# Performance work log

Hardware: AMD Instinct MI355X
Metric: run time of the kernel (lower is better)

The kernel has to match this reference:

```python
import jax, jax.numpy as jnp
import numpy as np

B, DC, DB, DF = 16384, 2048, 768, 256
NF = DB  # num_features (isSwinT=True)
EPS = 1e-5


def setup_inputs() -> dict:
    key = jax.random.key(0)
    ks = jax.random.split(key, 20)
    s = 0.02
    return {
        'x_context': jax.random.normal(ks[0], (B, DC), jnp.float32),
        'x_body': jax.random.normal(ks[1], (B, DB), jnp.float32),
        'x_face': jax.random.normal(ks[2], (B, DF), jnp.float32),
        'Wc': jax.random.normal(ks[3], (NF, DC), jnp.float32) * s,
        'bc': jax.random.normal(ks[4], (NF,), jnp.float32) * s,
        'Wa1': jax.random.normal(ks[5], (128, NF), jnp.float32) * s,
        'ba1': jax.random.normal(ks[6], (128,), jnp.float32) * s,
        'ga': jnp.ones((128,), jnp.float32),
        'bba': jnp.zeros((128,), jnp.float32),
        'Wa2': jax.random.normal(ks[7], (1, 128), jnp.float32) * s,
        'ba2': jax.random.normal(ks[8], (1,), jnp.float32) * s,
        'W1': jax.random.normal(ks[9], (256, NF * 3), jnp.float32) * s,
        'b1': jax.random.normal(ks[10], (256,), jnp.float32) * s,
        'g1': jnp.ones((256,), jnp.float32),
        'be1': jnp.zeros((256,), jnp.float32),
        'Wcat': jax.random.normal(ks[11], (26, 256), jnp.float32) * s,
        'bcat': jax.random.normal(ks[12], (26,), jnp.float32) * s,
    }


def _bn(x, g, b):
    # BatchNorm1d, training mode (biased batch stats), deterministic
    m = jnp.mean(x, axis=0)
    v = jnp.mean((x - m) ** 2, axis=0)
    return (x - m) * jax.lax.rsqrt(v + EPS) * g + b


def reference(x_context, x_body, x_face, Wc, bc, Wa1, ba1, ga, bba, Wa2, ba2,
              W1, b1, g1, be1, Wcat, bcat):
    # face repeated elementwise to body width: [B,256,1]->repeat(3)->view[B,768]
    face = jnp.repeat(x_face, DB // DF, axis=1)              # [B, NF]
    ctx = x_context @ Wc.T + bc                              # [B, NF]
    body = x_body                                            # [B, NF]

    def cross_atten(a, u, v):
        # two 1x1 dot-products, softmax over size-2 dim, weighted sum
        d = jnp.stack([jnp.sum(a * u, axis=1), jnp.sum(a * v, axis=1)], axis=1)  # [B,2]
        att = jax.nn.softmax(d, axis=1)
        # sum over dim2 of a[:, :, None] @ att[:, None, :] == a * att.sum(1)
        return a * jnp.sum(att, axis=1, keepdims=True)

    cfeat = cross_atten(ctx, body, face)
    bfeat = cross_atten(body, ctx, face)
    ffeat = cross_atten(face, ctx, body)

    def fc_att(x):
        h = _bn(x @ Wa1.T + ba1, ga, bba)
        h = jax.nn.gelu(h, approximate=False)
        return h @ Wa2.T + ba2                               # [B, 1]

    score = jax.nn.softmax(
        jnp.concatenate([fc_att(cfeat), fc_att(bfeat), fc_att(ffeat)], axis=1), axis=1)  # [B,3]
    cfeat = cfeat * score[:, 0:1]
    bfeat = bfeat * score[:, 1:2]
    ffeat = ffeat * score[:, 2:3]

    fuse = jnp.concatenate([cfeat, bfeat, ffeat], axis=1) @ W1.T + b1  # [B,256]
    fuse = jax.nn.relu(_bn(fuse, g1, be1))  # dropout p=0.5 treated as identity (eval)
    return fuse @ Wcat.T + bcat             # [B,26]
```

## Files before the change

kernel.cpp:

```cpp
#include <hip/hip_runtime.h>
#include <hip/hip_bf16.h>
#include <stdint.h>

typedef float f32x4 __attribute__((ext_vector_type(4)));
typedef short bf16x8 __attribute__((ext_vector_type(8)));
typedef unsigned short u16;

static constexpr int kB  = 16384;
static constexpr int kDC = 2048;
static constexpr int kNF = 768;
static constexpr float kEps = 1e-5f;

static constexpr size_t OFF_FEATS  = 0;
static constexpr size_t OFF_X      = 75497472;
static constexpr size_t OFF_WCBF   = OFF_X + 67108864;
static constexpr size_t OFF_WA1BF  = OFF_WCBF + 3145728;
static constexpr size_t OFF_W1BF   = OFF_WA1BF + 196608;
static constexpr size_t OFF_FUSE   = OFF_W1BF + 1179648;
static constexpr size_t OFF_SCORES = OFF_FUSE + 16777216;
static constexpr size_t OFF_STATS  = OFF_SCORES + 196608;

static __device__ __forceinline__ u16 f2bf(float x) {
  union { float f; unsigned u; } c; c.f = x;
  unsigned r = c.u + 0x7fffu + ((c.u >> 16) & 1u);
  return (u16)(r >> 16);
}

static __device__ __forceinline__ unsigned pk2(float lo, float hi) {
  union { __hip_bfloat162 h; unsigned u; } c;
  c.h = __float22bfloat162_rn(make_float2(lo, hi));
  return c.u;
}

static __device__ __forceinline__ void cvt4(const float* __restrict__ in, u16* __restrict__ out, long v) {
  const float4 f = ((const float4*)in)[v];
  ((ushort4*)out)[v] = make_ushort4(f2bf(f.x), f2bf(f.y), f2bf(f.z), f2bf(f.w));
}

__global__ __launch_bounds__(256) void prep_kernel(
    const float* __restrict__ xb, const float* __restrict__ xf,
    const float* __restrict__ Wc, const float* __restrict__ Wa1, const float* __restrict__ W1,
    u16* __restrict__ feats, u16* __restrict__ wcbf, u16* __restrict__ wa1bf, u16* __restrict__ w1bf)
{
  const int b = blockIdx.x, t = threadIdx.x;
  if (b < 3072) {
    const long base = (long)b * 1024 + t;
    u16* o = feats + (size_t)kB * kNF;
#pragma unroll
    for (int i = 0; i < 4; ++i) cvt4(xb, o, base + i * 256);
  } else if (b < 4096) {
    const long base = (long)(b - 3072) * 1024 + t;
#pragma unroll
    for (int i = 0; i < 4; ++i) {
      const long v = base + i * 256;
      const float4 f = ((const float4*)xf)[v];
      u16 e0 = f2bf(f.x), e1 = f2bf(f.y), e2 = f2bf(f.z), e3 = f2bf(f.w);
      size_t p = (size_t)v * 4;
      size_t row = p >> 8;
      int col = (int)(p & 255);
      u16* o = feats + (size_t)2 * kB * kNF + row * kNF + col * 3;
      ushort4* o4 = (ushort4*)o;
      o4[0] = make_ushort4(e0, e0, e0, e1);
      o4[1] = make_ushort4(e1, e1, e2, e2);
      o4[2] = make_ushort4(e2, e3, e3, e3);
    }
  } else if (b < 4480) {
    const long base = (long)(b - 4096) * 1024 + t;
#pragma unroll
    for (int i = 0; i < 4; ++i) cvt4(Wc, wcbf, base + i * 256);
  } else if (b < 4504) {
    const long base = (long)(b - 4480) * 1024 + t;
#pragma unroll
    for (int i = 0; i < 4; ++i) cvt4(Wa1, wa1bf, base + i * 256);
  } else {
    const long base = (long)(b - 4504) * 1024 + t;
#pragma unroll
    for (int i = 0; i < 4; ++i) cvt4(W1, w1bf, base + i * 256);
  }
}

static __device__ __forceinline__ void gload16(const void* g, void* l) {
  __builtin_amdgcn_global_load_lds(
      (const __attribute__((address_space(1))) void*)g,
      (__attribute__((address_space(3))) void*)l, 16, 0, 0);
}

__global__ __launch_bounds__(256) void gemm_a32(
    const float* __restrict__ A, const u16* __restrict__ B,
    const float* __restrict__ bias, u16* __restrict__ C)
{
  constexpr int APAD = 40;
  __shared__ __align__(16) u16 As[2 * 128 * APAD];
  __shared__ __align__(16) u16 Bs[2 * 128 * 32];
  const int bx = blockIdx.x, by = blockIdx.y;
  const size_t m0 = (size_t)bx * 128;
  const int n0 = by * 128;
  const int t = threadIdx.x;
  const int lane = t & 63, wave = t >> 6;
  const int wm = (wave >> 1) * 64, wn = (wave & 1) * 64;
  const int fr = lane & 15, fq = lane >> 4;

  const int srow = t >> 2, scol = (t & 3) * 8;
  const u16* gb0 = B + (size_t)(n0 + srow) * kDC + scol;
  const u16* gb1 = B + (size_t)(n0 + 64 + srow) * kDC + scol;

  const int arow = t >> 1, ah = (t & 1);
  const float* ga = A + (m0 + arow) * (size_t)kDC + ah * 16;
  const int lawoff = arow * APAD + ah * 16;

  float4 ra0, ra1, ra2, ra3;
  auto loadA = [&]() {
    ra0 = ((const float4*)ga)[0]; ra1 = ((const float4*)ga)[1];
    ra2 = ((const float4*)ga)[2]; ra3 = ((const float4*)ga)[3];
  };
  auto cvtWrite = [&](u16* dst) {
    uint4 w0, w1;
    w0.x = pk2(ra0.x, ra0.y); w0.y = pk2(ra0.z, ra0.w);
    w0.z = pk2(ra1.x, ra1.y); w0.w = pk2(ra1.z, ra1.w);
    w1.x = pk2(ra2.x, ra2.y); w1.y = pk2(ra2.z, ra2.w);
    w1.z = pk2(ra3.x, ra3.y); w1.w = pk2(ra3.z, ra3.w);
    ((uint4*)dst)[0] = w0; ((uint4*)dst)[1] = w1;
  };

  f32x4 acc[4][4] = {};

  loadA();
  cvtWrite(As + lawoff);
  gload16(gb0, Bs + t * 8);
  gload16(gb1, Bs + t * 8 + 2048);
  gb0 += 32; gb1 += 32;
  ga += 32; loadA();
  __syncthreads();

  for (int k = 0; k < 64; ++k) {
    const int cur = k & 1;
    if (k < 63) {
      u16* an = As + (cur ^ 1) * (128 * APAD);
      u16* bn = Bs + (cur ^ 1) * (128 * 32);
      cvtWrite(an + lawoff);
      gload16(gb0, bn + t * 8);
      gload16(gb1, bn + t * 8 + 2048);
      gb0 += 32; gb1 += 32;
      if (k < 62) { ga += 32; loadA(); }
    }
    const u16* fa = As + cur * (128 * APAD) + (wm + fr) * APAD + fq * 8;
    const u16* fb = Bs + cur * (128 * 32) + (wn + fr) * 32 + fq * 8;
    bf16x8 av[4], bv[4];
#pragma unroll
    for (int mf = 0; mf < 4; ++mf) av[mf] = *(const bf16x8*)(fa + mf * 16 * APAD);
#pragma unroll
    for (int nf = 0; nf < 4; ++nf) bv[nf] = *(const bf16x8*)(fb + nf * 512);
#pragma unroll
    for (int mf = 0; mf < 4; ++mf)
#pragma unroll
      for (int nf = 0; nf < 4; ++nf)
        acc[mf][nf] = __builtin_amdgcn_mfma_f32_16x16x32_bf16(av[mf], bv[nf], acc[mf][nf], 0, 0, 0);
    __syncthreads();
  }

#pragma unroll
  for (int mf = 0; mf < 4; ++mf) {
    const size_t rb = m0 + wm + mf * 16 + fq * 4;
#pragma unroll
    for (int nf = 0; nf < 4; ++nf) {
      const int gn = n0 + wn + nf * 16 + fr;
      const float bb = bias[gn];
#pragma unroll
      for (int rr = 0; rr < 4; ++rr)
        C[(rb + rr) * (size_t)kNF + gn] = f2bf(acc[mf][nf][rr] + bb);
    }
  }
}

template <int STATS>
__global__ __launch_bounds__(256) void gemm_bt64(
    const u16* __restrict__ A, int lda, const u16* __restrict__ B, int ldb,
    const float* __restrict__ bias, float* __restrict__ C, int ldc, int K,
    float* __restrict__ stats)
{
  __shared__ __align__(16) u16 As[2 * 64 * 32];
  __shared__ __align__(16) u16 Bs[2 * 128 * 32];
  const int bx = blockIdx.x, by = blockIdx.y;
  const size_t m0 = (size_t)bx * 64;
  const int n0 = by * 128;
  const int t = threadIdx.x;
  const int lane = t & 63, wave = t >> 6;
  const int wn = wave * 32;
  const int fr = lane & 15, fq = lane >> 4;

  const int srow = t >> 2, scol = (t & 3) * 8;
  const u16* ga0 = A + (m0 + srow) * (size_t)lda + scol;
  const u16* gb0 = B + (size_t)(n0 + srow) * ldb + scol;
  const u16* gb1 = B + (size_t)(n0 + 64 + srow) * ldb + scol;

  f32x4 acc[4][2] = {};

  gload16(ga0, As + t * 8);
  gload16(gb0, Bs + t * 8);
  gload16(gb1, Bs + t * 8 + 2048);
  ga0 += 32; gb0 += 32; gb1 += 32;
  __syncthreads();

  const int kt = K >> 5;
  for (int k = 0; k < kt; ++k) {
    const int cur = k & 1;
    if (k + 1 < kt) {
      u16* an = As + (cur ^ 1) * 2048;
      u16* bn = Bs + (cur ^ 1) * 4096;
      gload16(ga0, an + t * 8);
      gload16(gb0, bn + t * 8);
      gload16(gb1, bn + t * 8 + 2048);
      ga0 += 32; gb0 += 32; gb1 += 32;
    }
    const u16* fa = As + cur * 2048 + fr * 32 + fq * 8;
    const u16* fb = Bs + cur * 4096 + (wn + fr) * 32 + fq * 8;
    bf16x8 av[4], bv[2];
#pragma unroll
    for (int mf = 0; mf < 4; ++mf) av[mf] = *(const bf16x8*)(fa + mf * 512);
#pragma unroll
    for (int nf = 0; nf < 2; ++nf) bv[nf] = *(const bf16x8*)(fb + nf * 512);
#pragma unroll
    for (int mf = 0; mf < 4; ++mf)
#pragma unroll
      for (int nf = 0; nf < 2; ++nf)
        acc[mf][nf] = __builtin_amdgcn_mfma_f32_16x16x32_bf16(av[mf], bv[nf], acc[mf][nf], 0, 0, 0);
    __syncthreads();
  }

  float cs[2] = {}, cs2[2] = {};
#pragma unroll
  for (int mf = 0; mf < 4; ++mf) {
    const size_t rb = m0 + mf * 16 + fq * 4;
#pragma unroll
    for (int nf = 0; nf < 2; ++nf) {
      const int gn = n0 + wn + nf * 16 + fr;
      const float bb = bias[gn];
#pragma unroll
      for (int rr = 0; rr < 4; ++rr) {
        const float vv = acc[mf][nf][rr] + bb;
        C[(rb + rr) * (size_t)ldc + gn] = vv;
        if (STATS) { cs[nf] += vv; cs2[nf] += vv * vv; }
      }
    }
  }
  if (STATS) {
    const int f = (int)(m0 >> 14);
#pragma unroll
    for (int nf = 0; nf < 2; ++nf) {
      float s = cs[nf], s2 = cs2[nf];
      s += __shfl_down(s, 32); s2 += __shfl_down(s2, 32);
      s += __shfl_down(s, 16); s2 += __shfl_down(s2, 16);
      if (fq == 0) {
        const int gn = n0 + wn + nf * 16 + fr;
        atomicAdd(&stats[(f * 128 + gn) * 2 + 0], s);
        atomicAdd(&stats[(f * 128 + gn) * 2 + 1], s2);
      }
    }
  }
}

__global__ __launch_bounds__(256) void gemm_fuse64(
    const u16* __restrict__ feats, const u16* __restrict__ w1,
    const float* __restrict__ scores, const float* __restrict__ b1,
    float* __restrict__ fuse, float* __restrict__ fstats)
{
  __shared__ __align__(16) u16 As[2 * 64 * 32];
  __shared__ __align__(16) u16 Bs[2 * 128 * 32];
  const int bx = blockIdx.x, by = blockIdx.y;
  const size_t m0 = (size_t)bx * 64;
  const int n0 = by * 128;
  const int t = threadIdx.x;
  const int lane = t & 63, wave = t >> 6;
  const int wn = wave * 32;
  const int fr = lane & 15, fq = lane >> 4;
  const int srow = t >> 2, scol = (t & 3) * 8;

  const u16* ga0; const u16* gb0; const u16* gb1;
  auto setf = [&](int f) {
    ga0 = feats + (size_t)f * kB * kNF + (m0 + srow) * (size_t)kNF + scol;
    gb0 = w1 + f * kNF + (size_t)(n0 + srow) * 2304 + scol;
    gb1 = gb0 + (size_t)64 * 2304;
  };

  const f32x4 vzero = {};
  f32x4 acc[4][2] = {}, tot[4][2] = {};

  setf(0);
  gload16(ga0, As + t * 8);
  gload16(gb0, Bs + t * 8);
  gload16(gb1, Bs + t * 8 + 2048);
  ga0 += 32; gb0 += 32; gb1 += 32;
  int pf = 0, pk = 1;
  int ck = 0, cf = 0;
  __syncthreads();

  for (int s = 0; s < 72; ++s) {
    const int cur = s & 1;
    if (s < 71) {
      u16* an = As + (cur ^ 1) * 2048;
      u16* bn = Bs + (cur ^ 1) * 4096;
      gload16(ga0, an + t * 8);
      gload16(gb0, bn + t * 8);
      gload16(gb1, bn + t * 8 + 2048);
      if (++pk == 24) { pk = 0; ++pf; if (pf < 3) setf(pf); }
      else { ga0 += 32; gb0 += 32; gb1 += 32; }
    }
    const u16* fa = As + cur * 2048 + fr * 32 + fq * 8;
    const u16* fb = Bs + cur * 4096 + (wn + fr) * 32 + fq * 8;
    bf16x8 av[4], bv[2];
#pragma unroll
    for (int mf = 0; mf < 4; ++mf) av[mf] = *(const bf16x8*)(fa + mf * 512);
#pragma unroll
    for (int nf = 0; nf < 2; ++nf) bv[nf] = *(const bf16x8*)(fb + nf * 512);
#pragma unroll
    for (int mf = 0; mf < 4; ++mf)
#pragma unroll
      for (int nf = 0; nf < 2; ++nf)
        acc[mf][nf] = __builtin_amdgcn_mfma_f32_16x16x32_bf16(av[mf], bv[nf], acc[mf][nf], 0, 0, 0);
    if (++ck == 24) {
      ck = 0;
#pragma unroll
      for (int mf = 0; mf < 4; ++mf) {
        const size_t rb = m0 + mf * 16 + fq * 4;
#pragma unroll
        for (int rr = 0; rr < 4; ++rr) {
          const float sv = scores[(rb + rr) * 3 + cf];
#pragma unroll
          for (int nf = 0; nf < 2; ++nf) tot[mf][nf][rr] += sv * acc[mf][nf][rr];
        }
      }
#pragma unroll
      for (int mf = 0; mf < 4; ++mf)
#pragma unroll
        for (int nf = 0; nf < 2; ++nf) acc[mf][nf] = vzero;
      ++cf;
    }
    __syncthreads();
  }

  float cs[2] = {}, cs2[2] = {};
#pragma unroll
  for (int mf = 0; mf < 4; ++mf) {
    const size_t rb = m0 + mf * 16 + fq * 4;
#pragma unroll
    for (int nf = 0; nf < 2; ++nf) {
      const int gn = n0 + wn + nf * 16 + fr;
      const float bb = b1[gn];
#pragma unroll
      for (int rr = 0; rr < 4; ++rr) {
        const float vv = tot[mf][nf][rr] + bb;
        fuse[(rb + rr) * 256 + gn] = vv;
        cs[nf] += vv; cs2[nf] += vv * vv;
      }
    }
  }
#pragma unroll
  for (int nf = 0; nf < 2; ++nf) {
    float s = cs[nf], s2 = cs2[nf];
    s += __shfl_down(s, 32); s2 += __shfl_down(s2, 32);
    s += __shfl_down(s, 16); s2 += __shfl_down(s2, 16);
    if (fq == 0) {
      const int gn = n0 + wn + nf * 16 + fr;
      atomicAdd(&fstats[gn * 2 + 0], s);
      atomicAdd(&fstats[gn * 2 + 1], s2);
    }
  }
}

__global__ __launch_bounds__(64) void att_kernel(
    const float* __restrict__ H, const float* __restrict__ stats,
    const float* __restrict__ ga, const float* __restrict__ bba,
    const float* __restrict__ Wa2, const float* __restrict__ ba2,
    float* __restrict__ scores)
{
  const int i = blockIdx.x, l = threadIdx.x;
  float d[3];
#pragma unroll
  for (int f = 0; f < 3; ++f) {
    float part = 0.f;
#pragma unroll
    for (int h = 0; h < 2; ++h) {
      const int c = l + h * 64;
      const float sum = stats[(f * 128 + c) * 2 + 0];
      const float sq  = stats[(f * 128 + c) * 2 + 1];
      const float m = sum * (1.f / kB);
      const float var = sq * (1.f / kB) - m * m;
      const float rs = rsqrtf(var + kEps);
      const float x = H[((size_t)f * kB + i) * 128 + c];
      const float xn = (x - m) * rs * ga[c] + bba[c];
      const float ge = 0.5f * xn * (1.f + erff(xn * 0.70710678118f));
      part += ge * Wa2[c];
    }
#pragma unroll
    for (int off = 32; off > 0; off >>= 1) part += __shfl_down(part, off);
    d[f] = part;
  }
  if (l == 0) {
    const float b2 = ba2[0];
    float d0 = d[0] + b2, d1 = d[1] + b2, d2 = d[2] + b2;
    const float mx = fmaxf(d0, fmaxf(d1, d2));
    const float e0 = expf(d0 - mx), e1 = expf(d1 - mx), e2 = expf(d2 - mx);
    const float inv = 1.f / (e0 + e1 + e2);
    scores[i * 3 + 0] = e0 * inv;
    scores[i * 3 + 1] = e1 * inv;
    scores[i * 3 + 2] = e2 * inv;
  }
}

__global__ __launch_bounds__(64) void final_kernel(
    const float* __restrict__ fuse, const float* __restrict__ fstats,
    const float* __restrict__ g1, const float* __restrict__ be1,
    const float* __restrict__ Wcat, const float* __restrict__ bcat,
    float* __restrict__ out)
{
  const int i = blockIdx.x, l = threadIdx.x;
  __shared__ float row[256];
#pragma unroll
  for (int h = 0; h < 4; ++h) {
    const int c = l + h * 64;
    const float sum = fstats[c * 2 + 0], sq = fstats[c * 2 + 1];
    const float m = sum * (1.f / kB);
    const float var = sq * (1.f / kB) - m * m;
    const float rs = rsqrtf(var + kEps);
    const float v = (fuse[(size_t)i * 256 + c] - m) * rs * g1[c] + be1[c];
    row[c] = fmaxf(v, 0.f);
  }
  __syncthreads();
  if (l < 26) {
    float acc = bcat[l];
    const float* w = Wcat + l * 256;
    for (int k2 = 0; k2 < 256; ++k2) acc += row[k2] * w[k2];
    out[(size_t)i * 26 + l] = acc;
  }
}

extern "C" void kernel_launch(void* const* d_in, const int* in_sizes, int n_in,
                              void* d_out, int out_size, void* d_ws, size_t ws_size,
                              hipStream_t stream) {
  (void)in_sizes; (void)n_in; (void)out_size; (void)ws_size;
  const float* xc   = (const float*)d_in[0];
  const float* xb   = (const float*)d_in[1];
  const float* xf   = (const float*)d_in[2];
  const float* Wc   = (const float*)d_in[3];
  const float* bc   = (const float*)d_in[4];
  const float* Wa1  = (const float*)d_in[5];
  const float* ba1  = (const float*)d_in[6];
  const float* ga   = (const float*)d_in[7];
  const float* bba  = (const float*)d_in[8];
  const float* Wa2  = (const float*)d_in[9];
  const float* ba2  = (const float*)d_in[10];
  const float* W1   = (const float*)d_in[11];
  const float* b1   = (const float*)d_in[12];
  const float* g1   = (const float*)d_in[13];
  const float* be1  = (const float*)d_in[14];
  const float* Wcat = (const float*)d_in[15];
  const float* bcat = (const float*)d_in[16];
  float* out = (float*)d_out;

  char* ws = (char*)d_ws;
  u16* feats   = (u16*)(ws + OFF_FEATS);
  float* H     = (float*)(ws + OFF_X);
  u16* wcbf    = (u16*)(ws + OFF_WCBF);
  u16* wa1bf   = (u16*)(ws + OFF_WA1BF);
  u16* w1bf    = (u16*)(ws + OFF_W1BF);
  float* fuse  = (float*)(ws + OFF_FUSE);
  float* scores= (float*)(ws + OFF_SCORES);
  float* hst   = (float*)(ws + OFF_STATS);
  float* fst   = (float*)(ws + OFF_STATS + 3072);

  hipMemsetAsync(ws + OFF_STATS, 0, 5120, stream);
  prep_kernel<<<4648, 256, 0, stream>>>(xb, xf, Wc, Wa1, W1, feats, wcbf, wa1bf, w1bf);
  gemm_a32<<<dim3(128, 6), 256, 0, stream>>>(xc, wcbf, bc, feats);
  gemm_bt64<1><<<dim3(768, 1), 256, 0, stream>>>(feats, kNF, wa1bf, kNF, ba1, H, 128, kNF, hst);
  att_kernel<<<kB, 64, 0, stream>>>(H, hst, ga, bba, Wa2, ba2, scores);
  gemm_fuse64<<<dim3(256, 2), 256, 0, stream>>>(feats, w1bf, scores, b1, fuse, fst);
  final_kernel<<<kB, 64, 0, stream>>>(fuse, fst, g1, be1, Wcat, bcat, out);
}
```

Measured before the change: 299.8 us.

## Pre-convert x_context to bf16 and use single-buffered bf16 GEMM for context projection

Moves the fp32-to-bf16 conversion of x_context out of the context GEMM into the prep kernel, writing a bf16 copy into the workspace region later reused for H. The GEMM now loads both operands straight to LDS with global_load_lds and drops register-staged A conversion and double buffering. The prep kernel also doubles work per block. This adds an extra 128MB fp32 read plus 64MB bf16 write and read round trip, and the loss of double buffering may expose load latency.

```diff
diff --git a/kernel.cpp b/kernel.cpp
--- a/kernel.cpp
+++ b/kernel.cpp
@@ -26,32 +26,31 @@
   return (u16)(r >> 16);
 }
 
-static __device__ __forceinline__ unsigned pk2(float lo, float hi) {
-  union { __hip_bfloat162 h; unsigned u; } c;
-  c.h = __float22bfloat162_rn(make_float2(lo, hi));
-  return c.u;
-}
-
 static __device__ __forceinline__ void cvt4(const float* __restrict__ in, u16* __restrict__ out, long v) {
   const float4 f = ((const float4*)in)[v];
   ((ushort4*)out)[v] = make_ushort4(f2bf(f.x), f2bf(f.y), f2bf(f.z), f2bf(f.w));
 }
 
 __global__ __launch_bounds__(256) void prep_kernel(
-    const float* __restrict__ xb, const float* __restrict__ xf,
+    const float* __restrict__ xc, const float* __restrict__ xb, const float* __restrict__ xf,
     const float* __restrict__ Wc, const float* __restrict__ Wa1, const float* __restrict__ W1,
-    u16* __restrict__ feats, u16* __restrict__ wcbf, u16* __restrict__ wa1bf, u16* __restrict__ w1bf)
+    u16* __restrict__ axbf, u16* __restrict__ feats,
+    u16* __restrict__ wcbf, u16* __restrict__ wa1bf, u16* __restrict__ w1bf)
 {
   const int b = blockIdx.x, t = threadIdx.x;
-  if (b < 3072) {
-    const long base = (long)b * 1024 + t;
+  if (b < 4096) {
+    const long base = (long)b * 2048 + t;
+#pragma unroll
+    for (int i = 0; i < 8; ++i) cvt4(xc, axbf, base + i * 256);
+  } else if (b < 5632) {
+    const long base = (long)(b - 4096) * 2048 + t;
     u16* o = feats + (size_t)kB * kNF;
 #pragma unroll
-    for (int i = 0; i < 4; ++i) cvt4(xb, o, base + i * 256);
-  } else if (b < 4096) {
-    const long base = (long)(b - 3072) * 1024 + t;
-#pragma unroll
-    for (int i = 0; i < 4; ++i) {
+    for (int i = 0; i < 8; ++i) cvt4(xb, o, base + i * 256);
+  } else if (b < 6144) {
+    const long base = (long)(b - 5632) * 2048 + t;
+#pragma unroll
+    for (int i = 0; i < 8; ++i) {
       const long v = base + i * 256;
       const float4 f = ((const float4*)xf)[v];
       u16 e0 = f2bf(f.x), e1 = f2bf(f.y), e2 = f2bf(f.z), e3 = f2bf(f.w);
@@ -64,18 +63,18 @@
       o4[1] = make_ushort4(e1, e1, e2, e2);
       o4[2] = make_ushort4(e2, e3, e3, e3);
     }
-  } else if (b < 4480) {
-    const long base = (long)(b - 4096) * 1024 + t;
-#pragma unroll
-    for (int i = 0; i < 4; ++i) cvt4(Wc, wcbf, base + i * 256);
-  } else if (b < 4504) {
-    const long base = (long)(b - 4480) * 1024 + t;
-#pragma unroll
-    for (int i = 0; i < 4; ++i) cvt4(Wa1, wa1bf, base + i * 256);
+  } else if (b < 6336) {
+    const long base = (long)(b - 6144) * 2048 + t;
+#pragma unroll
+    for (int i = 0; i < 8; ++i) cvt4(Wc, wcbf, base + i * 256);
+  } else if (b < 6348) {
+    const long base = (long)(b - 6336) * 2048 + t;
+#pragma unroll
+    for (int i = 0; i < 8; ++i) cvt4(Wa1, wa1bf, base + i * 256);
   } else {
-    const long base = (long)(b - 4504) * 1024 + t;
-#pragma unroll
-    for (int i = 0; i < 4; ++i) cvt4(W1, w1bf, base + i * 256);
+    const long base = (long)(b - 6348) * 2048 + t;
+#pragma unroll
+    for (int i = 0; i < 8; ++i) cvt4(W1, w1bf, base + i * 256);
   }
 }
 
@@ -85,13 +84,12 @@
       (__attribute__((address_space(3))) void*)l, 16, 0, 0);
 }
 
-__global__ __launch_bounds__(256) void gemm_a32(
-    const float* __restrict__ A, const u16* __restrict__ B,
-    const float* __restrict__ bias, u16* __restrict__ C)
-{
-  constexpr int APAD = 40;
-  __shared__ __align__(16) u16 As[2 * 128 * APAD];
-  __shared__ __align__(16) u16 Bs[2 * 128 * 32];
+__global__ __launch_bounds__(256) void gemm_bt(
+    const u16* __restrict__ A, int lda, const u16* __restrict__ B, int ldb,
+    const float* __restrict__ bias, u16* __restrict__ C, int ldc, int K)
+{
+  __shared__ __align__(16) u16 As[128 * 32];
+  __shared__ __align__(16) u16 Bs[128 * 32];
   const int bx = blockIdx.x, by = blockIdx.y;
   const size_t m0 = (size_t)bx * 128;
   const int n0 = by * 128;
@@ -101,53 +99,29 @@
   const int fr = lane & 15, fq = lane >> 4;
 
   const int srow = t >> 2, scol = (t & 3) * 8;
-  const u16* gb0 = B + (size_t)(n0 + srow) * kDC + scol;
-  const u16* gb1 = B + (size_t)(n0 + 64 + srow) * kDC + scol;
-
-  const int arow = t >> 1, ah = (t & 1);
-  const float* ga = A + (m0 + arow) * (size_t)kDC + ah * 16;
-  const int lawoff = arow * APAD + ah * 16;
-
-  float4 ra0, ra1, ra2, ra3;
-  auto loadA = [&]() {
-    ra0 = ((const float4*)ga)[0]; ra1 = ((const float4*)ga)[1];
-    ra2 = ((const float4*)ga)[2]; ra3 = ((const float4*)ga)[3];
-  };
-  auto cvtWrite = [&](u16* dst) {
-    uint4 w0, w1;
-    w0.x = pk2(ra0.x, ra0.y); w0.y = pk2(ra0.z, ra0.w);
-    w0.z = pk2(ra1.x, ra1.y); w0.w = pk2(ra1.z, ra1.w);
-    w1.x = pk2(ra2.x, ra2.y); w1.y = pk2(ra2.z, ra2.w);
-    w1.z = pk2(ra3.x, ra3.y); w1.w = pk2(ra3.z, ra3.w);
-    ((uint4*)dst)[0] = w0; ((uint4*)dst)[1] = w1;
-  };
+  const u16* ga0 = A + (m0 + srow) * (size_t)lda + scol;
+  const u16* ga1 = A + (m0 + 64 + srow) * (size_t)lda + scol;
+  const u16* gb0 = B + (size_t)(n0 + srow) * ldb + scol;
+  const u16* gb1 = B + (size_t)(n0 + 64 + srow) * ldb + scol;
+  u16* la = As + t * 8;
+  u16* lb = Bs + t * 8;
+  const u16* fa = As + (wm + fr) * 32 + fq * 8;
+  const u16* fb = Bs + (wn + fr) * 32 + fq * 8;
 
   f32x4 acc[4][4] = {};
 
-  loadA();
-  cvtWrite(As + lawoff);
-  gload16(gb0, Bs + t * 8);
-  gload16(gb1, Bs + t * 8 + 2048);
-  gb0 += 32; gb1 += 32;
-  ga += 32; loadA();
-  __syncthreads();
-
-  for (int k = 0; k < 64; ++k) {
-    const int cur = k & 1;
-    if (k < 63) {
-      u16* an = As + (cur ^ 1) * (128 * APAD);
-      u16* bn = Bs + (cur ^ 1) * (128 * 32);
-      cvtWrite(an + lawoff);
-      gload16(gb0, bn + t * 8);
-      gload16(gb1, bn + t * 8 + 2048);
-      gb0 += 32; gb1 += 32;
-      if (k < 62) { ga += 32; loadA(); }
-    }
-    const u16* fa = As + cur * (128 * APAD) + (wm + fr) * APAD + fq * 8;
-    const u16* fb = Bs + cur * (128 * 32) + (wn + fr) * 32 + fq * 8;
+  const int kt = K >> 5;
+  for (int k = 0; k < kt; ++k) {
+    __syncthreads();
+    gload16(ga0, la);
+    gload16(ga1, la + 2048);
+    gload16(gb0, lb);
+    gload16(gb1, lb + 2048);
+    ga0 += 32; ga1 += 32; gb0 += 32; gb1 += 32;
+    __syncthreads();
     bf16x8 av[4], bv[4];
 #pragma unroll
-    for (int mf = 0; mf < 4; ++mf) av[mf] = *(const bf16x8*)(fa + mf * 16 * APAD);
+    for (int mf = 0; mf < 4; ++mf) av[mf] = *(const bf16x8*)(fa + mf * 512);
 #pragma unroll
     for (int nf = 0; nf < 4; ++nf) bv[nf] = *(const bf16x8*)(fb + nf * 512);
 #pragma unroll
@@ -155,7 +129,6 @@
 #pragma unroll
       for (int nf = 0; nf < 4; ++nf)
         acc[mf][nf] = __builtin_amdgcn_mfma_f32_16x16x32_bf16(av[mf], bv[nf], acc[mf][nf], 0, 0, 0);
-    __syncthreads();
   }
 
 #pragma unroll
@@ -167,7 +140,7 @@
       const float bb = bias[gn];
 #pragma unroll
       for (int rr = 0; rr < 4; ++rr)
-        C[(rb + rr) * (size_t)kNF + gn] = f2bf(acc[mf][nf][rr] + bb);
+        C[(rb + rr) * (size_t)ldc + gn] = f2bf(acc[mf][nf][rr] + bb);
     }
   }
 }
@@ -459,6 +432,7 @@
 
   char* ws = (char*)d_ws;
   u16* feats   = (u16*)(ws + OFF_FEATS);
+  u16* axbf    = (u16*)(ws + OFF_X);
   float* H     = (float*)(ws + OFF_X);
   u16* wcbf    = (u16*)(ws + OFF_WCBF);
   u16* wa1bf   = (u16*)(ws + OFF_WA1BF);
@@ -469,8 +443,8 @@
   float* fst   = (float*)(ws + OFF_STATS + 3072);
 
   hipMemsetAsync(ws + OFF_STATS, 0, 5120, stream);
-  prep_kernel<<<4648, 256, 0, stream>>>(xb, xf, Wc, Wa1, W1, feats, wcbf, wa1bf, w1bf);
-  gemm_a32<<<dim3(128, 6), 256, 0, stream>>>(xc, wcbf, bc, feats);
+  prep_kernel<<<6420, 256, 0, stream>>>(xc, xb, xf, Wc, Wa1, W1, axbf, feats, wcbf, wa1bf, w1bf);
+  gemm_bt<<<dim3(128, 6), 256, 0, stream>>>(axbf, kDC, wcbf, kDC, bc, feats, kNF, kDC);
   gemm_bt64<1><<<dim3(768, 1), 256, 0, stream>>>(feats, kNF, wa1bf, kNF, ba1, H, 128, kNF, hst);
   att_kernel<<<kB, 64, 0, stream>>>(H, hst, ga, bba, Wa2, ba2, scores);
   gemm_fuse64<<<dim3(256, 2), 256, 0, stream>>>(feats, w1bf, scores, b1, fuse, fst);
```

After: 300.8 us. About the same (+0.3%).
